# Optimization experiments

Hardware: AMD Instinct MI355X
Metric: run time of the kernel (lower is better)

The kernel has to match this reference:

```python
import jax, jax.numpy as jnp
import numpy as np
from jax import lax

BATCH, L, DM = 2, 2048, 1024
DI = 2 * DM          # d_inner
N = 16               # d_state
N2 = 2 * N           # augmented (and actual) state dim
K = 4                # d_conv
DTR = 64             # dt_rank = ceil(1024/16)
ALPHA = 0.1          # observer_alpha


def setup_inputs() -> dict:
    key = jax.random.key(0)
    ks = jax.random.split(key, 10)
    hidden_states = jax.random.normal(ks[0], (BATCH, L, DM), jnp.float32)
    in_proj_w = jax.random.normal(ks[1], (2 * DI, DM), jnp.float32) / np.sqrt(DM)
    conv_w = jax.random.normal(ks[2], (DI, K), jnp.float32) / np.sqrt(K)
    conv_b = jax.random.normal(ks[3], (DI,), jnp.float32) * 0.01
    x_proj_w = jax.random.normal(ks[4], (DTR + 2 * N2, DI), jnp.float32) / np.sqrt(DI)
    dt_init_std = DTR ** -0.5
    dt_proj_w = jax.random.uniform(ks[5], (DI, DTR), jnp.float32, -dt_init_std, dt_init_std)
    # dt bias init: inverse-softplus of dt ~ LogUniform(1e-3, 1e-1)
    dt = jnp.exp(jax.random.uniform(ks[6], (DI,), jnp.float32) * (np.log(0.1) - np.log(1e-3)) + np.log(1e-3))
    dt = jnp.clip(dt, 1e-4, None)
    dt_proj_b = dt + jnp.log(-jnp.expm1(-dt))
    # S4D-real init over the full (doubled) state dim, as in the torch module
    A_log = jnp.log(jnp.broadcast_to(jnp.arange(1, N2 + 1, dtype=jnp.float32), (DI, N2)))
    Dp = jnp.ones((DI,), jnp.float32)
    out_proj_w = jax.random.normal(ks[7], (DM, DI), jnp.float32) / np.sqrt(DI)
    observer_gain = jax.random.normal(ks[8], (N,), jnp.float32) * 0.01
    return dict(hidden_states=hidden_states, in_proj_w=in_proj_w, conv_w=conv_w,
                conv_b=conv_b, x_proj_w=x_proj_w, dt_proj_w=dt_proj_w,
                dt_proj_b=dt_proj_b, A_log=A_log, D=Dp, out_proj_w=out_proj_w,
                observer_gain=observer_gain)


def _mamba_observer_fwd(hidden_states, in_proj_w, conv_w, conv_b, x_proj_w,
                        dt_proj_w, dt_proj_b, A_log, D, out_proj_w, observer_gain):
    b, l, _ = hidden_states.shape
    # in_proj (no bias): (b, l, dm) -> (b, 2*di, l)
    xz = jnp.einsum('bld,ed->bel', hidden_states, in_proj_w)
    x, z = jnp.split(xz, 2, axis=1)  # (b, di, l) each
    # causal depthwise conv1d (kernel K, left pad K-1, truncate to L) + SiLU
    xp = jnp.pad(x, ((0, 0), (0, 0), (K - 1, 0)))
    x = sum(conv_w[None, :, i:i + 1] * xp[:, :, i:i + l] for i in range(K)) + conv_b[None, :, None]
    x = jax.nn.silu(x)
    # x_proj (no bias): (b, di, l) -> (b, l, dtr + 2*n2)
    x_dbl = jnp.einsum('bdl,ed->ble', x, x_proj_w)
    dt_low, Bm, Cm = jnp.split(x_dbl, [DTR, DTR + N2], axis=-1)  # (b,l,DTR),(b,l,N2),(b,l,N2)
    delta = jax.nn.softplus(jnp.einsum('blr,dr->bld', dt_low, dt_proj_w) + dt_proj_b)  # (b,l,di)
    # observer augmentation: take first N columns, build 2N-state diagonal SSM
    A = -jnp.exp(A_log)            # (di, N2)
    A16 = A[:, :N]
    gamma = jax.nn.softplus(observer_gain)  # (N,)
    A_aug = jnp.concatenate([A16, A16 - gamma[None, :]], axis=1)  # (di, N2)
    Bo = Bm[..., :N]
    Co = Cm[..., :N]
    B_aug = jnp.concatenate([Bo, Bo + gamma * D.mean()], axis=-1)        # (b,l,N2)
    C_aug = jnp.concatenate([(1.0 - ALPHA) * Co, ALPHA * Co], axis=-1)   # (b,l,N2)
    u = jnp.moveaxis(x, 2, 1)  # (b, l, di)
    # selective scan over l with carried state (b, di, N2)
    def step(state, inp):
        delta_t, B_t, C_t, u_t = inp  # (b,di),(b,N2),(b,N2),(b,di)
        dA = jnp.exp(delta_t[:, :, None] * A_aug[None])            # (b,di,N2)
        state = state * dA + (delta_t * u_t)[:, :, None] * B_t[:, None, :]
        y_t = jnp.einsum('bdn,bn->bd', state, C_t)
        return state, y_t
    xs = (jnp.moveaxis(delta, 1, 0), jnp.moveaxis(B_aug, 1, 0),
          jnp.moveaxis(C_aug, 1, 0), jnp.moveaxis(u, 1, 0))
    init = jnp.zeros((b, DI, N2), hidden_states.dtype)
    _, ys = lax.scan(step, init, xs)          # (l, b, di)
    y = jnp.moveaxis(ys, 0, 1)                # (b, l, di)
    y = y + D[None, None, :] * u
    y = y * jax.nn.silu(jnp.moveaxis(z, 2, 1))
    return jnp.einsum('bld,od->blo', y, out_proj_w)  # (b, l, dm)


def reference(hidden_states, in_proj_w, conv_w, conv_b, x_proj_w, dt_proj_w,
              dt_proj_b, A_log, D, out_proj_w, observer_gain):
    return _mamba_observer_fwd(hidden_states, in_proj_w, conv_w, conv_b, x_proj_w,
                               dt_proj_w, dt_proj_b, A_log, D, out_proj_w, observer_gain)
```

## Files before the change

### kernel.cpp

```cpp
#include <hip/hip_runtime.h>
#include <math.h>

#define LSEQ   2048
#define DMODEL 1024
#define DI     2048
#define NST    32
#define CH     32
#define NCH    64
#define LOG2E  1.44269504f

typedef __attribute__((ext_vector_type(8))) short   short8;
typedef __attribute__((ext_vector_type(2))) float   floatx2;
typedef __attribute__((ext_vector_type(4))) float   floatx4;
typedef __attribute__((ext_vector_type(8))) float   floatx8;
typedef __attribute__((ext_vector_type(8))) __bf16  bfx8;

#if __has_builtin(__builtin_amdgcn_exp2f)
#define EXP2F __builtin_amdgcn_exp2f
#else
#define EXP2F exp2f
#endif

__device__ __forceinline__ float softplusf(float x) {
  return (x > 20.f) ? x : log1pf(__expf(x));
}
__device__ __forceinline__ float siluf(float x) {
  return x / (1.f + __expf(-x));
}

__device__ __forceinline__ void async_copy16(const void* g, void* l) {
  __builtin_amdgcn_global_load_lds(
      (const __attribute__((address_space(1))) void*)g,
      (__attribute__((address_space(3))) void*)l, 16, 0, 0);
}

__global__ __launch_bounds__(256) void prep_inputs(
    const float* __restrict__ hs, const float* __restrict__ ipw,
    const float* __restrict__ xpw, const float* __restrict__ opw,
    const float* __restrict__ dtw, const float* __restrict__ D,
    short* __restrict__ hs_bf, short* __restrict__ ipw_bf,
    short* __restrict__ xw96_bf, short* __restrict__ opw_bf,
    short* __restrict__ dtw_bf, float* __restrict__ dmean)
{
  __shared__ float red[256];
  const int blk = blockIdx.x;
  const int tid = threadIdx.x;
  if (blk < 2048) {
    long long i = ((long long)blk * 256 + tid) * 8;
    floatx8 f = *(const floatx8*)&hs[i];
    bfx8 b = __builtin_convertvector(f, bfx8);
    *(short8*)&hs_bf[i] = *(short8*)&b;
  } else if (blk < 4096) {
    long long i = ((long long)(blk - 2048) * 256 + tid) * 8;
    floatx8 f = *(const floatx8*)&ipw[i];
    bfx8 b = __builtin_convertvector(f, bfx8);
    *(short8*)&ipw_bf[i] = *(short8*)&b;
  } else if (blk < 5120) {
    long long i = ((long long)(blk - 4096) * 256 + tid) * 8;
    floatx8 f = *(const floatx8*)&opw[i];
    bfx8 b = __builtin_convertvector(f, bfx8);
    *(short8*)&opw_bf[i] = *(short8*)&b;
  } else if (blk < 5248) {
    long long j = ((long long)(blk - 5120) * 256 + tid) * 8;
    int row = (int)(j >> 11);
    int k   = (int)(j & 2047);
    if (row < 96) {
      int sr = (row < 80) ? row : row + 16;
      floatx8 f = *(const floatx8*)&xpw[(long long)sr * DI + k];
      bfx8 b = __builtin_convertvector(f, bfx8);
      *(short8*)&xw96_bf[j] = *(short8*)&b;
    } else {
      *(short8*)&xw96_bf[j] = (short8){0,0,0,0,0,0,0,0};
    }
  } else if (blk < 5312) {
    long long i = ((long long)(blk - 5248) * 256 + tid) * 8;
    floatx8 f = *(const floatx8*)&dtw[i];
    bfx8 b = __builtin_convertvector(f, bfx8);
    *(short8*)&dtw_bf[i] = *(short8*)&b;
  } else {
    float s = 0.f;
    for (int i = tid; i < DI; i += 256) s += D[i];
    red[tid] = s; __syncthreads();
    for (int off = 128; off > 0; off >>= 1) {
      if (tid < off) red[tid] += red[tid + off];
      __syncthreads();
    }
    if (tid == 0) dmean[0] = red[0] * (1.f / (float)DI);
  }
}

__global__ __launch_bounds__(256) void gemm_inproj_bf16(
    const short* __restrict__ A, const short* __restrict__ B, __bf16* __restrict__ C,
    int Kd, int ldc, long long Bbatch, long long Cbatch)
{
  const int bid = blockIdx.x;
  const int xcd = bid & 7;
  const int j   = bid >> 3;
  const int mt  = j >> 2;
  const int t   = j & 3;
  const int nt  = xcd * 2 + (t & 1);
  const int bz  = t >> 1;
  B += bz * Bbatch;
  C += bz * Cbatch;
  const int m0 = mt * 64;
  const int n0 = nt * 128;

  __shared__ short As[64 * 32];
  __shared__ short Bs[128 * 32];
  const int tid  = threadIdx.x;
  const int lane = tid & 63;
  const int wave = tid >> 6;
  const int wm = (wave & 1) * 32;
  const int wn = (wave >> 1) * 64;
  const int fm = lane & 15;
  const int quad = lane >> 4;
  const int fk = quad * 8;

  floatx4 acc[2][4];
  #pragma unroll
  for (int i = 0; i < 2; ++i)
    #pragma unroll
    for (int jj = 0; jj < 4; ++jj) acc[i][jj] = (floatx4){0.f, 0.f, 0.f, 0.f};

  const int r0 = tid >> 2;
  const int kc0 = (tid & 3) * 8;

  for (int k0 = 0; k0 < Kd; k0 += 32) {
    __syncthreads();
    async_copy16(&A[(long long)(m0 + r0) * Kd + k0 + kc0], &As[tid * 8]);
    async_copy16(&B[(long long)(n0 + r0) * Kd + k0 + kc0], &Bs[tid * 8]);
    async_copy16(&B[(long long)(n0 + r0 + 64) * Kd + k0 + kc0], &Bs[(tid + 256) * 8]);
    __syncthreads();
    short8 af[2], bf[4];
    #pragma unroll
    for (int i = 0; i < 2; ++i) af[i] = *(const short8*)&As[(wm + i * 16 + fm) * 32 + fk];
    #pragma unroll
    for (int jj = 0; jj < 4; ++jj) bf[jj] = *(const short8*)&Bs[(wn + jj * 16 + fm) * 32 + fk];
    #pragma unroll
    for (int i = 0; i < 2; ++i)
      #pragma unroll
      for (int jj = 0; jj < 4; ++jj)
        acc[i][jj] = __builtin_amdgcn_mfma_f32_16x16x32_bf16(af[i], bf[jj], acc[i][jj], 0, 0, 0);
  }

  #pragma unroll
  for (int i = 0; i < 2; ++i)
    #pragma unroll
    for (int jj = 0; jj < 4; ++jj)
      #pragma unroll
      for (int r = 0; r < 4; ++r) {
        int row = m0 + wm + i * 16 + quad * 4 + r;
        int col = n0 + wn + jj * 16 + fm;
        C[(long long)row * ldc + col] = (__bf16)acc[i][jj][r];
      }
}

__global__ __launch_bounds__(256) void gemm_outproj_bf16(
    const short* __restrict__ A, const short* __restrict__ B, float* __restrict__ C)
{
  const int bid = blockIdx.x;
  const int xcd = bid & 7;
  const int j   = bid >> 3;
  const int nt  = j & 7;
  const int mt  = xcd * 8 + (j >> 3);
  const int m0 = mt * 64;
  const int n0 = nt * 128;

  __shared__ short As[64 * 32];
  __shared__ short Bs[128 * 32];
  const int tid  = threadIdx.x;
  const int lane = tid & 63;
  const int wave = tid >> 6;
  const int wm = (wave & 1) * 32;
  const int wn = (wave >> 1) * 64;
  const int fm = lane & 15;
  const int quad = lane >> 4;
  const int fk = quad * 8;

  floatx4 acc[2][4];
  #pragma unroll
  for (int i = 0; i < 2; ++i)
    #pragma unroll
    for (int jj = 0; jj < 4; ++jj) acc[i][jj] = (floatx4){0.f, 0.f, 0.f, 0.f};

  const int r0 = tid >> 2;
  const int kc0 = (tid & 3) * 8;

  for (int k0 = 0; k0 < DI; k0 += 32) {
    __syncthreads();
    async_copy16(&A[(long long)(m0 + r0) * DI + k0 + kc0], &As[tid * 8]);
    async_copy16(&B[(long long)(n0 + r0) * DI + k0 + kc0], &Bs[tid * 8]);
    async_copy16(&B[(long long)(n0 + r0 + 64) * DI + k0 + kc0], &Bs[(tid + 256) * 8]);
    __syncthreads();
    short8 af[2], bf[4];
    #pragma unroll
    for (int i = 0; i < 2; ++i) af[i] = *(const short8*)&As[(wm + i * 16 + fm) * 32 + fk];
    #pragma unroll
    for (int jj = 0; jj < 4; ++jj) bf[jj] = *(const short8*)&Bs[(wn + jj * 16 + fm) * 32 + fk];
    #pragma unroll
    for (int i = 0; i < 2; ++i)
      #pragma unroll
      for (int jj = 0; jj < 4; ++jj)
        acc[i][jj] = __builtin_amdgcn_mfma_f32_16x16x32_bf16(af[i], bf[jj], acc[i][jj], 0, 0, 0);
  }

  #pragma unroll
  for (int i = 0; i < 2; ++i)
    #pragma unroll
    for (int jj = 0; jj < 4; ++jj)
      #pragma unroll
      for (int r = 0; r < 4; ++r) {
        int row = m0 + wm + i * 16 + quad * 4 + r;
        int col = n0 + wn + jj * 16 + fm;
        C[(long long)row * DMODEL + col] = acc[i][jj][r];
      }
}

__global__ __launch_bounds__(256) void gemm_dtproj_bf16(
    const short* __restrict__ A, const short* __restrict__ B,
    const float* __restrict__ dtb, __bf16* __restrict__ delta)
{
  const int m0 = blockIdx.y * 64;
  const int n0 = blockIdx.x * 128;
  __shared__ short As[64 * 32];
  __shared__ short Bs[128 * 32];
  const int tid  = threadIdx.x;
  const int lane = tid & 63;
  const int wave = tid >> 6;
  const int wm = (wave & 1) * 32;
  const int wn = (wave >> 1) * 64;
  const int fm = lane & 15;
  const int quad = lane >> 4;
  const int fk = quad * 8;

  floatx4 acc[2][4];
  #pragma unroll
  for (int i = 0; i < 2; ++i)
    #pragma unroll
    for (int jj = 0; jj < 4; ++jj) acc[i][jj] = (floatx4){0.f, 0.f, 0.f, 0.f};

  const int r0 = tid >> 2;
  const int kc0 = (tid & 3) * 8;

  #pragma unroll
  for (int k0 = 0; k0 < 64; k0 += 32) {
    __syncthreads();
    async_copy16(&A[(long long)(m0 + r0) * 64 + k0 + kc0], &As[tid * 8]);
    async_copy16(&B[(long long)(n0 + r0) * 64 + k0 + kc0], &Bs[tid * 8]);
    async_copy16(&B[(long long)(n0 + r0 + 64) * 64 + k0 + kc0], &Bs[(tid + 256) * 8]);
    __syncthreads();
    short8 af[2], bf[4];
    #pragma unroll
    for (int i = 0; i < 2; ++i) af[i] = *(const short8*)&As[(wm + i * 16 + fm) * 32 + fk];
    #pragma unroll
    for (int jj = 0; jj < 4; ++jj) bf[jj] = *(const short8*)&Bs[(wn + jj * 16 + fm) * 32 + fk];
    #pragma unroll
    for (int i = 0; i < 2; ++i)
      #pragma unroll
      for (int jj = 0; jj < 4; ++jj)
        acc[i][jj] = __builtin_amdgcn_mfma_f32_16x16x32_bf16(af[i], bf[jj], acc[i][jj], 0, 0, 0);
  }

  #pragma unroll
  for (int jj = 0; jj < 4; ++jj) {
    int col = n0 + wn + jj * 16 + fm;
    float bias = dtb[col];
    #pragma unroll
    for (int i = 0; i < 2; ++i)
      #pragma unroll
      for (int r = 0; r < 4; ++r) {
        int row = m0 + wm + i * 16 + quad * 4 + r;
        delta[(long long)row * DI + col] = (__bf16)softplusf(acc[i][jj][r] + bias);
      }
  }
}

__global__ __launch_bounds__(256) void gemm_xproj_bf16(
    const short* __restrict__ A, const short* __restrict__ B, float* __restrict__ Cp)
{
  const int m0 = blockIdx.x * 128;
  const int ks = blockIdx.y;
  const int kb = ks * 256;
  __shared__ short As[128 * 32];
  __shared__ short Bs[128 * 32];
  const int tid  = threadIdx.x;
  const int lane = tid & 63;
  const int wave = tid >> 6;
  const int wm = (wave & 1) * 64;
  const int wn = (wave >> 1) * 64;
  const int fm = lane & 15;
  const int fk = (lane >> 4) * 8;

  floatx4 acc[4][4];
  #pragma unroll
  for (int i = 0; i < 4; ++i)
    #pragma unroll
    for (int j = 0; j < 4; ++j) acc[i][j] = (floatx4){0.f, 0.f, 0.f, 0.f};

  const int r0 = tid >> 2;
  const int kc0 = (tid & 3) * 8;

  for (int k0 = kb; k0 < kb + 256; k0 += 32) {
    __syncthreads();
    async_copy16(&A[(long long)(m0 + r0) * DI + k0 + kc0], &As[tid * 8]);
    async_copy16(&A[(long long)(m0 + r0 + 64) * DI + k0 + kc0], &As[(tid + 256) * 8]);
    async_copy16(&B[(long long)r0 * DI + k0 + kc0], &Bs[tid * 8]);
    async_copy16(&B[(long long)(r0 + 64) * DI + k0 + kc0], &Bs[(tid + 256) * 8]);
    __syncthreads();
    short8 af[4], bf[4];
    #pragma unroll
    for (int i = 0; i < 4; ++i) af[i] = *(const short8*)&As[(wm + i * 16 + fm) * 32 + fk];
    #pragma unroll
    for (int j = 0; j < 4; ++j) bf[j] = *(const short8*)&Bs[(wn + j * 16 + fm) * 32 + fk];
    #pragma unroll
    for (int i = 0; i < 4; ++i)
      #pragma unroll
      for (int j = 0; j < 4; ++j)
        acc[i][j] = __builtin_amdgcn_mfma_f32_16x16x32_bf16(af[i], bf[j], acc[i][j], 0, 0, 0);
  }

  float* Co = Cp + (long long)ks * (4096LL * 128);
  const int quad = lane >> 4;
  #pragma unroll
  for (int i = 0; i < 4; ++i)
    #pragma unroll
    for (int j = 0; j < 4; ++j)
      #pragma unroll
      for (int r = 0; r < 4; ++r) {
        int row = m0 + wm + i * 16 + quad * 4 + r;
        int col = wn + j * 16 + fm;
        Co[(long long)row * 128 + col] = acc[i][j][r];
      }
}

__global__ __launch_bounds__(256) void conv_silu_transpose(
    const __bf16* __restrict__ xz, const float* __restrict__ conv_w,
    const float* __restrict__ conv_b, __bf16* __restrict__ u, __bf16* __restrict__ zt)
{
  const int b  = blockIdx.z;
  const int l0 = blockIdx.x * 32;
  const int e0 = blockIdx.y * 32;
  __shared__ float tile[32][33];
  const int tx = threadIdx.x, ty = threadIdx.y;
  const __bf16* src = xz + ((long long)b * 4096 + e0) * LSEQ;
  #pragma unroll
  for (int i = 0; i < 4; ++i) {
    int el = ty + i * 8;
    int e  = e0 + el;
    int l  = l0 + tx;
    const __bf16* row = src + (long long)el * LSEQ;
    float v;
    if (e < DI) {
      float s = conv_b[e];
      #pragma unroll
      for (int kk = 0; kk < 4; ++kk) {
        int li = l - 3 + kk;
        float xv = (li >= 0) ? (float)row[li] : 0.f;
        s = fmaf(conv_w[e * 4 + kk], xv, s);
      }
      v = s;
    } else {
      v = (float)row[l];
    }
    tile[el][tx] = siluf(v);
  }
  __syncthreads();
  __bf16* dst = (e0 < DI) ? (u + (long long)b * LSEQ * DI)
                          : (zt + (long long)b * LSEQ * DI);
  const int ecol = (e0 < DI) ? e0 : e0 - DI;
  #pragma unroll
  for (int i = 0; i < 4; ++i) {
    int lr = ty + i * 8;
    int l  = l0 + lr;
    dst[(long long)l * DI + ecol + tx] = (__bf16)tile[tx][lr];
  }
}

__global__ __launch_bounds__(256) void prep_k(
    const float* __restrict__ partial, const float* __restrict__ og,
    const float* __restrict__ dmean_p,
    float* __restrict__ Baug, float* __restrict__ Caug,
    short* __restrict__ dtlow_bf)
{
  const int blk = blockIdx.x;
  if (blk < 512) {
    const int tid = blk * 256 + threadIdx.x;
    const float dmean = *dmean_p;
    const int n = tid & 31;
    const int bl = tid >> 5;
    const int nn = n & 15;
    const float gamma = softplusf(og[nn]);
    float Bo = 0.f, Co = 0.f;
    #pragma unroll
    for (int ks = 0; ks < 8; ++ks) {
      const float* p = &partial[(long long)ks * (4096LL * 128) + (long long)bl * 128];
      Bo += p[64 + nn];
      Co += p[80 + nn];
    }
    Baug[tid] = (n < 16) ? Bo : Bo + gamma * dmean;
    Caug[tid] = (n < 16) ? 0.9f * Co : 0.1f * Co;
  } else {
    const int g = (blk - 512) * 256 + threadIdx.x;
    const int bl = g >> 6;
    const int r  = g & 63;
    float s = 0.f;
    #pragma unroll
    for (int ks = 0; ks < 8; ++ks)
      s += partial[(long long)ks * (4096LL * 128) + (long long)bl * 128 + r];
    __bf16 v = (__bf16)s;
    dtlow_bf[(long long)bl * 64 + r] = *(short*)&v;
  }
}

__global__ __launch_bounds__(256) void scan_phase1(
    const __bf16* __restrict__ delta, const __bf16* __restrict__ u,
    const float* __restrict__ Baug, const float* __restrict__ og,
    float* __restrict__ dtsum, __bf16* __restrict__ Q)
{
  const int d  = blockIdx.x * 256 + threadIdx.x;
  const int c  = blockIdx.y;
  const int b  = blockIdx.z;
  const int t0 = c * CH;
  __shared__ float Bsm[CH][NST];
  __shared__ float gsh[16];
  const int tid = threadIdx.x;
  {
    int row = tid >> 3;
    int kq  = (tid & 7) << 2;
    *(float4*)&Bsm[row][kq] =
        *(const float4*)&Baug[((long long)b * LSEQ + t0 + row) * NST + kq];
  }
  if (tid < 16) gsh[tid] = softplusf(og[tid]);
  __syncthreads();
  float gam[16];
  #pragma unroll
  for (int i = 0; i < 4; ++i) *(float4*)&gam[i * 4] = *(const float4*)&gsh[i * 4];

  floatx2 s2[8], so2[8];
  #pragma unroll
  for (int i = 0; i < 8; ++i) { s2[i] = (floatx2){0.f, 0.f}; so2[i] = (floatx2){0.f, 0.f}; }
  float dts = 0.f;
  const __bf16* dptr = delta + ((long long)b * LSEQ + t0) * DI + d;
  const __bf16* uptr = u     + ((long long)b * LSEQ + t0) * DI + d;
  for (int t = 0; t < CH; ++t) {
    float dt = (float)dptr[(long long)t * DI];
    float ut = (float)uptr[(long long)t * DI];
    dts += dt;
    float du  = dt * ut;
    float dt2 = dt * LOG2E;
    float E   = EXP2F(-dt2);
    float E2  = E * E;
    floatx2 a   = {E, E2};
    const floatx2 e22 = {E2, E2};
    const floatx2 du2 = {du, du};
    #pragma unroll
    for (int i = 0; i < 8; ++i) {
      floatx2 bl = *(const floatx2*)&Bsm[t][2 * i];
      floatx2 bh = *(const floatx2*)&Bsm[t][16 + 2 * i];
      floatx2 eg = {EXP2F(-dt2 * gam[2 * i]), EXP2F(-dt2 * gam[2 * i + 1])};
      s2[i]  = s2[i] * a + du2 * bl;
      floatx2 a2 = a * eg;
      so2[i] = so2[i] * a2 + du2 * bh;
      a = a * e22;
    }
  }
  dtsum[((long long)b * NCH + c) * DI + d] = dts;
  const long long qb = ((long long)b * NCH + c) * NST * DI + d;
  #pragma unroll
  for (int i = 0; i < 8; ++i) {
    Q[qb + (long long)(2 * i) * DI]          = (__bf16)s2[i].x;
    Q[qb + (long long)(2 * i + 1) * DI]      = (__bf16)s2[i].y;
    Q[qb + (long long)(16 + 2 * i) * DI]     = (__bf16)so2[i].x;
    Q[qb + (long long)(16 + 2 * i + 1) * DI] = (__bf16)so2[i].y;
  }
}

__global__ __launch_bounds__(256) void scan_phase2(
    const float* __restrict__ dtsum, const float* __restrict__ og,
    __bf16* __restrict__ Q)
{
  const int g = blockIdx.x * 256 + threadIdx.x;
  const int d = g & (DI - 1);
  const int n = (g >> 11) & (NST - 1);
  const int b = g >> 16;
  const int nn = n & 15;
  float k = (float)(nn + 1);
  if (n >= 16) k += softplusf(og[nn]);
  k *= LOG2E;
  float S = 0.f;
  for (int c = 0; c < NCH; ++c) {
    long long qidx = (((long long)b * NCH + c) * NST + n) * (long long)DI + d;
    float ds = dtsum[((long long)b * NCH + c) * DI + d];
    float q = (float)Q[qidx];
    Q[qidx] = (__bf16)S;
    S = fmaf(EXP2F(-ds * k), S, q);
  }
}

__global__ __launch_bounds__(256) void scan_phase3(
    const __bf16* __restrict__ delta, const __bf16* __restrict__ u,
    const __bf16* __restrict__ zt,
    const float* __restrict__ Baug, const float* __restrict__ Caug,
    const float* __restrict__ og, const __bf16* __restrict__ Sinit,
    const float* __restrict__ Dp, __bf16* __restrict__ ybf)
{
  const int d  = blockIdx.x * 256 + threadIdx.x;
  const int c  = blockIdx.y;
  const int b  = blockIdx.z;
  const int t0 = c * CH;
  __shared__ float Bsm[CH][NST];
  __shared__ float Csm[CH][NST];
  __shared__ float gsh[16];
  const int tid = threadIdx.x;
  {
    int row = tid >> 3;
    int kq  = (tid & 7) << 2;
    *(float4*)&Bsm[row][kq] =
        *(const float4*)&Baug[((long long)b * LSEQ + t0 + row) * NST + kq];
    *(float4*)&Csm[row][kq] =
        *(const float4*)&Caug[((long long)b * LSEQ + t0 + row) * NST + kq];
  }
  if (tid < 16) gsh[tid] = softplusf(og[tid]);
  __syncthreads();
  float gam[16];
  #pragma unroll
  for (int i = 0; i < 4; ++i) *(float4*)&gam[i * 4] = *(const float4*)&gsh[i * 4];

  floatx2 s2[8], so2[8];
  const long long qb = ((long long)b * NCH + c) * NST * DI + d;
  #pragma unroll
  for (int i = 0; i < 8; ++i) {
    s2[i]  = (floatx2){(float)Sinit[qb + (long long)(2 * i) * DI],
                       (float)Sinit[qb + (long long)(2 * i + 1) * DI]};
    so2[i] = (floatx2){(float)Sinit[qb + (long long)(16 + 2 * i) * DI],
                       (float)Sinit[qb + (long long)(16 + 2 * i + 1) * DI]};
  }
  const float Dd = Dp[d];

  const __bf16* dptr = delta + ((long long)b * LSEQ + t0) * DI + d;
  const __bf16* uptr = u     + ((long long)b * LSEQ + t0) * DI + d;
  const __bf16* zptr = zt    + ((long long)b * LSEQ + t0) * DI + d;
  __bf16*       yptr = ybf   + ((long long)b * LSEQ + t0) * DI + d;
  for (int t = 0; t < CH; ++t) {
    float dt = (float)dptr[(long long)t * DI];
    float ut = (float)uptr[(long long)t * DI];
    float du  = dt * ut;
    float dt2 = dt * LOG2E;
    float E   = EXP2F(-dt2);
    float E2  = E * E;
    floatx2 a   = {E, E2};
    const floatx2 e22 = {E2, E2};
    const floatx2 du2 = {du, du};
    floatx2 yl = {0.f, 0.f}, yh = {0.f, 0.f};
    #pragma unroll
    for (int i = 0; i < 8; ++i) {
      floatx2 bl = *(const floatx2*)&Bsm[t][2 * i];
      floatx2 bh = *(const floatx2*)&Bsm[t][16 + 2 * i];
      floatx2 cl = *(const floatx2*)&Csm[t][2 * i];
      floatx2 ch = *(const floatx2*)&Csm[t][16 + 2 * i];
      floatx2 eg = {EXP2F(-dt2 * gam[2 * i]), EXP2F(-dt2 * gam[2 * i + 1])};
      s2[i]  = s2[i] * a + du2 * bl;
      yl = yl + s2[i] * cl;
      floatx2 a2 = a * eg;
      so2[i] = so2[i] * a2 + du2 * bh;
      yh = yh + so2[i] * ch;
      a = a * e22;
    }
    float yv = yl.x + yl.y + yh.x + yh.y;
    yv = fmaf(Dd, ut, yv);
    float g = (float)zptr[(long long)t * DI];
    yptr[(long long)t * DI] = (__bf16)(yv * g);
  }
}

extern "C" void kernel_launch(void* const* d_in, const int* in_sizes, int n_in,
                              void* d_out, int out_size, void* d_ws, size_t ws_size,
                              hipStream_t stream) {
  const float* hs   = (const float*)d_in[0];
  const float* ipw  = (const float*)d_in[1];
  const float* cw   = (const float*)d_in[2];
  const float* cb   = (const float*)d_in[3];
  const float* xpw  = (const float*)d_in[4];
  const float* dtw  = (const float*)d_in[5];
  const float* dtbv = (const float*)d_in[6];
  const float* Dp   = (const float*)d_in[8];
  const float* opw  = (const float*)d_in[9];
  const float* og   = (const float*)d_in[10];
  float* out = (float*)d_out;
  float* ws  = (float*)d_ws;

  __bf16* xz_bf  = (__bf16*)ws;
  __bf16* delta  = (__bf16*)ws;
  __bf16* ybf    = (__bf16*)(ws + 4194304);
  __bf16* Qbuf   = (__bf16*)(ws + 8388608);
  short* hs_bf   = (short*)(ws + 16777216);
  short* ipw_bf  = (short*)(ws + 18874368);
  __bf16* u_bf   = (__bf16*)(ws + 16777216);
  __bf16* z_bf   = (__bf16*)(ws + 20971520);
  float* partial = ws + 25165824;
  float* dtsum   = ws + 25165824;
  float* Baug    = ws + 29753344;
  float* Caug    = ws + 29884416;
  float* dmean   = ws + 30015488;
  short* xw96_bf = (short*)(ws + 30015496);
  short* opw_bf  = (short*)(ws + 30146568);
  short* dtlow_bf = (short*)(ws + 31195144);
  short* dtw_bf   = (short*)(ws + 31326216);

  prep_inputs<<<5313, 256, 0, stream>>>(hs, ipw, xpw, opw, dtw, Dp,
                                        hs_bf, ipw_bf, xw96_bf, opw_bf, dtw_bf, dmean);

  gemm_inproj_bf16<<<2048, 256, 0, stream>>>(
      ipw_bf, hs_bf, xz_bf, DMODEL, LSEQ,
      (long long)LSEQ * DMODEL, (long long)4096 * LSEQ);

  conv_silu_transpose<<<dim3(64, 128, 2), dim3(32, 8), 0, stream>>>(xz_bf, cw, cb, u_bf, z_bf);

  gemm_xproj_bf16<<<dim3(32, 8), 256, 0, stream>>>((const short*)u_bf, xw96_bf, partial);

  prep_k<<<1536, 256, 0, stream>>>(partial, og, dmean, Baug, Caug, dtlow_bf);

  gemm_dtproj_bf16<<<dim3(16, 64), 256, 0, stream>>>(
      dtlow_bf, dtw_bf, dtbv, delta);

  scan_phase1<<<dim3(8, NCH, 2), 256, 0, stream>>>(delta, u_bf, Baug, og, dtsum, Qbuf);
  scan_phase2<<<512, 256, 0, stream>>>(dtsum, og, Qbuf);
  scan_phase3<<<dim3(8, NCH, 2), 256, 0, stream>>>(delta, u_bf, z_bf, Baug, Caug, og, Qbuf, Dp, ybf);

  gemm_outproj_bf16<<<512, 256, 0, stream>>>(
      (const short*)ybf, opw_bf, out);
}
```

Measured before the change: 362.6 us.

## Rewrite in-proj GEMM with 256x256 tiles, double-buffered swizzled LDS

Replaces the 64x128-tile in-projection GEMM with a 256x256-tile kernel of 512 threads. It double-buffers the K=64 stages so the async global-to-LDS copies of the next tile overlap the MFMA work on the current one. An XOR swizzle on the LDS layout is meant to avoid bank conflicts. The larger tiles raise operand reuse and cut global traffic and barrier count. The cost is 128KB of LDS per block, which allows only one block per CU, and a grid of just 256 blocks with no batch-stride parameters.

```diff
diff --git a/kernel.cpp b/kernel.cpp
--- a/kernel.cpp
+++ b/kernel.cpp
@@ -89,69 +89,95 @@
   }
 }
 
-__global__ __launch_bounds__(256) void gemm_inproj_bf16(
-    const short* __restrict__ A, const short* __restrict__ B, __bf16* __restrict__ C,
-    int Kd, int ldc, long long Bbatch, long long Cbatch)
+__global__ __launch_bounds__(512, 2) void gemm_inproj256(
+    const short* __restrict__ A,
+    const short* __restrict__ B,
+    __bf16* __restrict__ C)
 {
   const int bid = blockIdx.x;
   const int xcd = bid & 7;
   const int j   = bid >> 3;
-  const int mt  = j >> 2;
-  const int t   = j & 3;
-  const int nt  = xcd * 2 + (t & 1);
-  const int bz  = t >> 1;
-  B += bz * Bbatch;
-  C += bz * Cbatch;
-  const int m0 = mt * 64;
-  const int n0 = nt * 128;
-
-  __shared__ short As[64 * 32];
-  __shared__ short Bs[128 * 32];
+  const int nt  = xcd * 2 + (j & 1);
+  const int mt  = j >> 1;
+  const int m0 = mt * 256;
+  const int n0 = nt * 256;
+
+  __shared__ short As[2][256 * 64];
+  __shared__ short Bs[2][256 * 64];
+
   const int tid  = threadIdx.x;
   const int lane = tid & 63;
   const int wave = tid >> 6;
-  const int wm = (wave & 1) * 32;
-  const int wn = (wave >> 1) * 64;
+  const int wm = (wave >> 2) * 128;
+  const int wn = (wave & 3) * 64;
   const int fm = lane & 15;
   const int quad = lane >> 4;
-  const int fk = quad * 8;
-
-  floatx4 acc[2][4];
-  #pragma unroll
-  for (int i = 0; i < 2; ++i)
+
+  floatx4 acc[8][4];
+  #pragma unroll
+  for (int i = 0; i < 8; ++i)
     #pragma unroll
     for (int jj = 0; jj < 4; ++jj) acc[i][jj] = (floatx4){0.f, 0.f, 0.f, 0.f};
 
-  const int r0 = tid >> 2;
-  const int kc0 = (tid & 3) * 8;
-
-  for (int k0 = 0; k0 < Kd; k0 += 32) {
+  #define STAGE_IP(buf, kt)                                                   \
+    {                                                                         \
+      const int k0s = (kt) * 64;                                              \
+      _Pragma("unroll")                                                       \
+      for (int q = 0; q < 4; ++q) {                                           \
+        int o  = q * 8192 + tid * 16;                                         \
+        int sr = o >> 7;                                                      \
+        int sc = (o & 127) ^ ((sr & 7) << 4);                                 \
+        async_copy16(&A[((long long)(m0 + sr) << 10) + k0s + (sc >> 1)],      \
+                     (char*)&As[buf][0] + o);                                 \
+        async_copy16(&B[((long long)(n0 + sr) << 10) + k0s + (sc >> 1)],      \
+                     (char*)&Bs[buf][0] + o);                                 \
+      }                                                                       \
+    }
+
+  STAGE_IP(0, 0);
+  __syncthreads();
+
+  for (int t = 0; t < 16; ++t) {
+    const int cur = t & 1;
+    if (t < 15) STAGE_IP(cur ^ 1, t + 1);
+    #pragma unroll
+    for (int kk = 0; kk < 2; ++kk) {
+      const int colb = kk * 64 + quad * 16;
+      short8 af[8], bf[4];
+      #pragma unroll
+      for (int i = 0; i < 8; ++i) {
+        int row = wm + i * 16 + fm;
+        af[i] = *(const short8*)((const char*)&As[cur][0] +
+                                 (row << 7) + (colb ^ ((row & 7) << 4)));
+      }
+      #pragma unroll
+      for (int jj = 0; jj < 4; ++jj) {
+        int row = wn + jj * 16 + fm;
+        bf[jj] = *(const short8*)((const char*)&Bs[cur][0] +
+                                  (row << 7) + (colb ^ ((row & 7) << 4)));
+      }
+      #pragma unroll
+      for (int i = 0; i < 8; ++i)
+        #pragma unroll
+        for (int jj = 0; jj < 4; ++jj)
+          acc[i][jj] = __builtin_amdgcn_mfma_f32_16x16x32_bf16(af[i], bf[jj], acc[i][jj], 0, 0, 0);
+    }
     __syncthreads();
-    async_copy16(&A[(long long)(m0 + r0) * Kd + k0 + kc0], &As[tid * 8]);
-    async_copy16(&B[(long long)(n0 + r0) * Kd + k0 + kc0], &Bs[tid * 8]);
-    async_copy16(&B[(long long)(n0 + r0 + 64) * Kd + k0 + kc0], &Bs[(tid + 256) * 8]);
-    __syncthreads();
-    short8 af[2], bf[4];
-    #pragma unroll
-    for (int i = 0; i < 2; ++i) af[i] = *(const short8*)&As[(wm + i * 16 + fm) * 32 + fk];
-    #pragma unroll
-    for (int jj = 0; jj < 4; ++jj) bf[jj] = *(const short8*)&Bs[(wn + jj * 16 + fm) * 32 + fk];
-    #pragma unroll
-    for (int i = 0; i < 2; ++i)
-      #pragma unroll
-      for (int jj = 0; jj < 4; ++jj)
-        acc[i][jj] = __builtin_amdgcn_mfma_f32_16x16x32_bf16(af[i], bf[jj], acc[i][jj], 0, 0, 0);
-  }
-
-  #pragma unroll
-  for (int i = 0; i < 2; ++i)
+  }
+  #undef STAGE_IP
+
+  const int bz = n0 >> 11;
+  const int nb = n0 & 2047;
+  __bf16* Cb = C + (long long)bz * 4096 * 2048;
+  #pragma unroll
+  for (int i = 0; i < 8; ++i)
     #pragma unroll
     for (int jj = 0; jj < 4; ++jj)
       #pragma unroll
       for (int r = 0; r < 4; ++r) {
         int row = m0 + wm + i * 16 + quad * 4 + r;
-        int col = n0 + wn + jj * 16 + fm;
-        C[(long long)row * ldc + col] = (__bf16)acc[i][jj][r];
+        int col = nb + wn + jj * 16 + fm;
+        Cb[(long long)row * 2048 + col] = (__bf16)acc[i][jj][r];
       }
 }
 
@@ -610,9 +636,7 @@
   prep_inputs<<<5313, 256, 0, stream>>>(hs, ipw, xpw, opw, dtw, Dp,
                                         hs_bf, ipw_bf, xw96_bf, opw_bf, dtw_bf, dmean);
 
-  gemm_inproj_bf16<<<2048, 256, 0, stream>>>(
-      ipw_bf, hs_bf, xz_bf, DMODEL, LSEQ,
-      (long long)LSEQ * DMODEL, (long long)4096 * LSEQ);
+  gemm_inproj256<<<256, 512, 0, stream>>>(ipw_bf, hs_bf, xz_bf);
 
   conv_silu_transpose<<<dim3(64, 128, 2), dim3(32, 8), 0, stream>>>(xz_bf, cw, cb, u_bf, z_bf);
 
```

Measured after the change: 349.7 us. -3.6%, faster.
